# Kernel tuning notes

Measured on AMD Instinct MI355X. Metric: run time of the kernel, lower is better.

Reference implementation:

```python
import jax, jax.numpy as jnp
import numpy as np

D_MODEL = 768
D_STATE = 64
D_CONV = 4
EXPAND = 2
D_INNER = D_MODEL * EXPAND
BATCH = 2
SEQ = 1024
LN_EPS = 1e-5


def setup_inputs() -> dict:
    key = jax.random.key(0)
    ks = jax.random.split(key, 8)
    s = lambda k, shape, scale=0.02: (jax.random.normal(k, shape, jnp.float32) * scale)
    x = jax.random.normal(ks[0], (BATCH, SEQ, D_MODEL), jnp.float32)
    return {
        "x": x,
        "ln_w": jnp.ones((D_MODEL,), jnp.float32),
        "ln_b": jnp.zeros((D_MODEL,), jnp.float32),
        "in_proj_w": s(ks[1], (D_MODEL, 2 * D_INNER)),            # x @ W, torch Linear weight transposed
        "conv_w": s(ks[2], (D_INNER, 1, D_CONV), 0.1),            # depthwise (O, I/groups=1, K)
        "conv_b": jnp.zeros((D_INNER,), jnp.float32),
        "x_proj_w": s(ks[3], (D_INNER, 2 * D_STATE + 1)),
        "A_log": jnp.log(jnp.arange(1, D_STATE + 1, dtype=jnp.float32)),
        "D": jnp.ones((D_INNER,), jnp.float32),
        "dt_w": s(ks[4], (1, D_INNER), 0.5),
        "dt_b": s(ks[5], (D_INNER,), 0.1),
        "out_proj_w": s(ks[6], (D_INNER, D_MODEL)),
    }


def reference(x, ln_w, ln_b, in_proj_w, conv_w, conv_b, x_proj_w, A_log, D, dt_w, dt_b, out_proj_w):
    residual = x
    # LayerNorm
    mu = jnp.mean(x, axis=-1, keepdims=True)
    var = jnp.mean((x - mu) ** 2, axis=-1, keepdims=True)
    h = (x - mu) * jax.lax.rsqrt(var + LN_EPS) * ln_w + ln_b
    # input projection -> (main, gate)
    xz = h @ in_proj_w                                   # (B, L, 2*d_inner)
    x_main, z = jnp.split(xz, 2, axis=-1)
    # causal depthwise conv1d: torch pads (d_conv-1) both sides then truncates to L == left-pad only
    xc = jax.lax.conv_general_dilated(
        x_main.transpose(0, 2, 1), conv_w,
        window_strides=(1,), padding=[(D_CONV - 1, 0)],
        feature_group_count=D_INNER,
        dimension_numbers=("NCH", "OIH", "NCH"))
    xc = (xc + conv_b[None, :, None]).transpose(0, 2, 1)  # (B, L, d_inner)
    xc = jax.nn.silu(xc)
    # input-dependent SSM params
    proj = xc @ x_proj_w                                  # (B, L, 2*d_state+1)
    Bm = proj[..., :D_STATE]
    Cm = proj[..., D_STATE:2 * D_STATE]
    dt = jax.nn.softplus(proj[..., -1:] @ dt_w + dt_b)    # (B, L, d_inner)
    A = -jnp.exp(A_log)                                   # (d_state,)

    def step(h_prev, inp):
        x_t, dt_t, B_t, C_t = inp                         # (B,d_inner),(B,d_inner),(B,d_state),(B,d_state)
        dA = jnp.exp(A[None, None, :] * dt_t[..., None])  # (B, d_inner, d_state)
        h_new = dA * h_prev + (dt_t * x_t)[..., None] * B_t[:, None, :]
        y_t = jnp.einsum("bds,bs->bd", h_new, C_t)
        return h_new, y_t

    h0 = jnp.zeros((x.shape[0], D_INNER, D_STATE), xc.dtype)
    xs = (xc.transpose(1, 0, 2), dt.transpose(1, 0, 2),
          Bm.transpose(1, 0, 2), Cm.transpose(1, 0, 2))
    _, ys = jax.lax.scan(step, h0, xs)                    # ys: (L, B, d_inner)
    y = ys.transpose(1, 0, 2)
    y = y + D * xc
    y = y * jax.nn.silu(z)
    y = y @ out_proj_w                                    # (B, L, d_model)
    return y + residual
```

## Files before the change

kernel.cpp:

```cpp
#include <hip/hip_runtime.h>
#include <hip/hip_bf16.h>
#include <cstdint>
#include <cstddef>

#define D_MODEL   768
#define D_INNER   1536
#define D_STATE   64
#define NBATCH    2
#define SEQ       1024
#define NROWS     (NBATCH*SEQ)
#define NCHUNK    64
#define TCHUNK    16
#define PROJ_LD   132
#define BD_TOT    (NBATCH*D_INNER)

#define L2E 1.4426950408889634f
#define LN2 0.6931471805599453f

typedef __bf16 bf16x8 __attribute__((ext_vector_type(8)));
typedef float  f32x4  __attribute__((ext_vector_type(4)));

__device__ __forceinline__ float fexp2(float x){ return __builtin_amdgcn_exp2f(x); }
__device__ __forceinline__ float flog2(float x){ return __builtin_amdgcn_logf(x); }
__device__ __forceinline__ float softplus_f(float x){
  float r = LN2 * flog2(1.0f + fexp2(x * L2E));
  return x > 15.0f ? x : r;
}
__device__ __forceinline__ float silu_f(float x){
  return x / (1.0f + fexp2(-x * L2E));
}

__device__ __forceinline__ void gload_lds16(const void* g, void* l){
  __builtin_amdgcn_global_load_lds(
      (const __attribute__((address_space(1))) void*)g,
      (__attribute__((address_space(3))) void*)l, 16, 0, 0);
}

#define T1_TILES 2304
#define T3_TILES 1152
#define T2_TILES 192
#define TP_TOTAL (T1_TILES+T3_TILES+T2_TILES)

__global__ __launch_bounds__(256) void prep_all_kernel(
    const float* __restrict__ in_proj, const float* __restrict__ out_proj,
    const float* __restrict__ x_proj, const float* __restrict__ x,
    const float* __restrict__ ln_w, const float* __restrict__ ln_b,
    __bf16* __restrict__ WT1, __bf16* __restrict__ WT3,
    __bf16* __restrict__ WT2, __bf16* __restrict__ h_ln){
  __shared__ float shbuf[32*33];
  const int blk = blockIdx.x;
  if (blk < TP_TOTAL){
    const float* W; __bf16* WT; int K, ldw, tiles_x, idx;
    if (blk < T1_TILES){ W = in_proj; WT = WT1; K = D_MODEL; ldw = 2*D_INNER; tiles_x = 96; idx = blk; }
    else if (blk < T1_TILES+T3_TILES){ W = out_proj; WT = WT3; K = D_INNER; ldw = D_MODEL; tiles_x = 24; idx = blk - T1_TILES; }
    else { W = x_proj; WT = WT2; K = D_INNER; ldw = 129; tiles_x = 4; idx = blk - T1_TILES - T3_TILES; }
    const int n0 = (idx % tiles_x) * 32, k0 = (idx / tiles_x) * 32;
    const int tx = threadIdx.x, ty = threadIdx.y;
    float (*tile)[33] = (float(*)[33])shbuf;
    #pragma unroll
    for (int i = ty; i < 32; i += 8)
      tile[i][tx] = W[(size_t)(k0 + i) * ldw + n0 + tx];
    __syncthreads();
    #pragma unroll
    for (int i = ty; i < 32; i += 8)
      WT[(size_t)(n0 + i) * K + k0 + tx] = (__bf16)tile[tx][i];
  } else {
    const int row = blk - TP_TOTAL;
    const float* xr = x + (size_t)row * D_MODEL;
    const int tid = threadIdx.y * 32 + threadIdx.x;
    float v0 = xr[tid], v1 = xr[tid+256], v2 = xr[tid+512];
    float s  = v0+v1+v2;
    float ss = v0*v0+v1*v1+v2*v2;
    #pragma unroll
    for (int off = 32; off > 0; off >>= 1){
      s  += __shfl_down(s, off);
      ss += __shfl_down(ss, off);
    }
    float* red = shbuf;
    const int wv = tid >> 6, ln = tid & 63;
    if (ln == 0){ red[wv] = s; red[4+wv] = ss; }
    __syncthreads();
    if (tid == 0){
      float S  = red[0]+red[1]+red[2]+red[3];
      float SS = red[4]+red[5]+red[6]+red[7];
      float mu = S * (1.0f/D_MODEL);
      float var = SS * (1.0f/D_MODEL) - mu*mu;
      red[0] = mu;
      red[1] = rsqrtf(var + 1e-5f);
    }
    __syncthreads();
    float mu = red[0], inv = red[1];
    __bf16* orow = h_ln + (size_t)row * D_MODEL;
    orow[tid]     = (__bf16)((v0 - mu)*inv*ln_w[tid]     + ln_b[tid]);
    orow[tid+256] = (__bf16)((v1 - mu)*inv*ln_w[tid+256] + ln_b[tid+256]);
    orow[tid+512] = (__bf16)((v2 - mu)*inv*ln_w[tid+512] + ln_b[tid+512]);
  }
}

struct SMem {
  __bf16 sA[128][32];
  __bf16 sB[128][32];
};

template<int MODE>
__device__ __forceinline__ void gemm_tile(
    const __bf16* __restrict__ A, const __bf16* __restrict__ Bt,
    float* __restrict__ C,
    int lda, int ldb, int ldc, int m0, int n0, int kbeg, int kend,
    SMem& sm, int tid){
  const int wave = tid >> 6;
  const int lane = tid & 63;
  const int quad = lane >> 4;
  const int l16  = lane & 15;
  const int wm = (wave >> 1) * 64;
  const int wn = (wave & 1) * 64;
  const int srow = lane >> 2;
  const int scol = (lane & 3) * 8;

  f32x4 acc[4][4] = {};
  for (int k0 = kbeg; k0 < kend; k0 += 32){
    #pragma unroll
    for (int p = 0; p < 2; ++p){
      int r = wave*32 + p*16 + srow;
      gload_lds16(A  + (size_t)(m0 + r)*lda + k0 + scol, &sm.sA[wave*32 + p*16][0]);
      gload_lds16(Bt + (size_t)(n0 + r)*ldb + k0 + scol, &sm.sB[wave*32 + p*16][0]);
    }
    __syncthreads();
    bf16x8 af[4], bfr[4];
    #pragma unroll
    for (int i = 0; i < 4; ++i) af[i]  = *(const bf16x8*)&sm.sA[wm + i*16 + l16][quad*8];
    #pragma unroll
    for (int j = 0; j < 4; ++j) bfr[j] = *(const bf16x8*)&sm.sB[wn + j*16 + l16][quad*8];
    #pragma unroll
    for (int i = 0; i < 4; ++i)
      #pragma unroll
      for (int j = 0; j < 4; ++j)
        acc[i][j] = __builtin_amdgcn_mfma_f32_16x16x32_bf16(af[i], bfr[j], acc[i][j], 0, 0, 0);
    __syncthreads();
  }
  #pragma unroll
  for (int i = 0; i < 4; ++i)
    #pragma unroll
    for (int j = 0; j < 4; ++j)
      #pragma unroll
      for (int r = 0; r < 4; ++r){
        int row = m0 + wm + i*16 + quad*4 + r;
        int col = n0 + wn + j*16 + l16;
        size_t off = (size_t)row * ldc + col;
        if (MODE == 2) atomicAdd(&C[off], acc[i][j][r]);
        else           C[off] = acc[i][j][r];
      }
}

struct Args {
  const __bf16* h_ln; const __bf16* WT1; const __bf16* WT2; const __bf16* WT3;
  const float* conv_w; const float* conv_b; const float* x_proj;
  const float* dt_w; const float* dt_b; const float* Dp; const float* x;
  float* xz; float* xc; __bf16* xcb; float* proj;
  float* dtv; float* dtx;
  float* sdtA; __bf16* Lb; __bf16* ybf; float* out;
};

__global__ __launch_bounds__(256) void k_gemm1(Args a){
  __shared__ SMem sm;
  gemm_tile<0>(a.h_ln, a.WT1, a.xz, D_MODEL, D_MODEL, 2*D_INNER,
               blockIdx.y*128, blockIdx.x*128, 0, D_MODEL, sm, threadIdx.x);
}

__global__ __launch_bounds__(256) void k_conv(Args a){
  __shared__ float red[4];
  const int row = blockIdx.x;
  const int t   = row & (SEQ-1);
  const int tid = threadIdx.x;
  float vq[6];
  float dtpart = 0.0f;
  #pragma unroll
  for (int q = 0; q < 6; ++q){
    const int d = tid + q*256;
    const float4 w4 = *(const float4*)(a.conv_w + (size_t)d*4);
    float acc = a.conv_b[d];
    if (t >= 3) acc = fmaf(a.xz[(size_t)(row-3)*(2*D_INNER) + d], w4.x, acc);
    if (t >= 2) acc = fmaf(a.xz[(size_t)(row-2)*(2*D_INNER) + d], w4.y, acc);
    if (t >= 1) acc = fmaf(a.xz[(size_t)(row-1)*(2*D_INNER) + d], w4.z, acc);
    acc = fmaf(a.xz[(size_t)row*(2*D_INNER) + d], w4.w, acc);
    float v = silu_f(acc);
    vq[q] = v;
    a.xc[(size_t)row*D_INNER + d]  = v;
    a.xcb[(size_t)row*D_INNER + d] = (__bf16)v;
    dtpart = fmaf(v, a.x_proj[(size_t)d*129 + 128], dtpart);
  }
  #pragma unroll
  for (int off = 32; off > 0; off >>= 1) dtpart += __shfl_down(dtpart, off);
  const int wv = tid >> 6, ln = tid & 63;
  if (ln == 0) red[wv] = dtpart;
  __syncthreads();
  const float draw = red[0]+red[1]+red[2]+red[3];
  #pragma unroll
  for (int q = 0; q < 6; ++q){
    const int d = tid + q*256;
    float dv = softplus_f(fmaf(draw, a.dt_w[d], a.dt_b[d]));
    a.dtv[(size_t)row*D_INNER + d] = dv;
    a.dtx[(size_t)row*D_INNER + d] = dv * vq[q];
  }
  if (tid < 128) a.proj[(size_t)row * PROJ_LD + tid] = 0.0f;
  const float* xr = a.x + (size_t)row * D_MODEL;
  float* orow = a.out + (size_t)row * D_MODEL;
  orow[tid]     = xr[tid];
  orow[tid+256] = xr[tid+256];
  orow[tid+512] = xr[tid+512];
}

__global__ __launch_bounds__(256) void k_xproj(Args a){
  __shared__ SMem sm;
  const int kz = blockIdx.x;
  const int m0 = blockIdx.y * 128;
  gemm_tile<2>(a.xcb, a.WT2, a.proj, D_INNER, D_INNER, PROJ_LD,
               m0, 0, kz*384, kz*384+384, sm, threadIdx.x);
}


__global__ __launch_bounds__(256) void k_scanA(Args a){
  const int half = blockIdx.x & 1;
  const int bd = (blockIdx.x >> 1) * 256 + threadIdx.x;
  const int c  = blockIdx.y;
  const int b  = __builtin_amdgcn_readfirstlane(bd / D_INNER);
  const int d  = bd - b * D_INNER;
  float h[32];
  #pragma unroll
  for (int n = 0; n < 32; ++n) h[n] = 0.0f;
  float sdt = 0.0f;
  #pragma unroll 2
  for (int tl = 0; tl < TCHUNK; ++tl){
    const int row = b*SEQ + c*TCHUNK + tl;
    const float* Brow = a.proj + (size_t)row * PROJ_LD + half*32;
    float dtv = a.dtv[(size_t)row * D_INNER + d];
    float dtx = a.dtx[(size_t)row * D_INNER + d];
    sdt += dtv;
    float r1 = fexp2(-L2E * dtv);
    float r2 = r1*r1, r4 = r2*r2, r8 = r4*r4;
    float r16 = r8*r8, r32 = r16*r16;
    float base = half ? r32 : 1.0f;
    float p0=r1*base, p1=r2*base, p2=r1*r2*base, p3=r4*base,
          p4=r1*r4*base, p5=r2*r4*base, p6=r1*r2*r4*base, p7=r8*base;
    #pragma unroll
    for (int n = 0; n < 32; n += 8){
      h[n]   = fmaf(p0, h[n],   dtx * Brow[n]);
      h[n+1] = fmaf(p1, h[n+1], dtx * Brow[n+1]);
      h[n+2] = fmaf(p2, h[n+2], dtx * Brow[n+2]);
      h[n+3] = fmaf(p3, h[n+3], dtx * Brow[n+3]);
      h[n+4] = fmaf(p4, h[n+4], dtx * Brow[n+4]);
      h[n+5] = fmaf(p5, h[n+5], dtx * Brow[n+5]);
      h[n+6] = fmaf(p6, h[n+6], dtx * Brow[n+6]);
      h[n+7] = fmaf(p7, h[n+7], dtx * Brow[n+7]);
      if (n + 8 < 32){
        p0*=r8; p1*=r8; p2*=r8; p3*=r8; p4*=r8; p5*=r8; p6*=r8; p7*=r8;
      }
    }
  }
  if (half == 0) a.sdtA[(size_t)c * BD_TOT + bd] = sdt;
  #pragma unroll
  for (int n = 0; n < 32; ++n)
    a.Lb[((size_t)c * D_STATE + half*32 + n) * BD_TOT + bd] = (__bf16)h[n];
}

__global__ __launch_bounds__(256) void k_scanB(Args a){
  const int bd = blockIdx.x * 256 + threadIdx.x;
  const int n  = blockIdx.y;
  const float k2n = -(float)(n+1) * L2E;
  float h = 0.0f;
  #pragma unroll 4
  for (int c = 0; c < NCHUNK; ++c){
    float sdt = a.sdtA[(size_t)c * BD_TOT + bd];
    float P = fexp2(k2n * sdt);
    size_t adr = ((size_t)c * D_STATE + n) * BD_TOT + bd;
    float L = (float)a.Lb[adr];
    a.Lb[adr] = (__bf16)h;
    h = fmaf(P, h, L);
  }
}

__global__ __launch_bounds__(256) void k_scanC(Args a){
  const int bd = blockIdx.x * 256 + threadIdx.x;
  const int c  = blockIdx.y;
  const int b  = __builtin_amdgcn_readfirstlane(bd / D_INNER);
  const int d  = bd - b * D_INNER;
  const float Dd = a.Dp[d];
  float h[D_STATE];
  #pragma unroll
  for (int n = 0; n < D_STATE; ++n)
    h[n] = (float)a.Lb[((size_t)c * D_STATE + n) * BD_TOT + bd];
  #pragma unroll 2
  for (int tl = 0; tl < TCHUNK; ++tl){
    const int row = b*SEQ + c*TCHUNK + tl;
    const float* Brow = a.proj + (size_t)row * PROJ_LD;
    const float* Crow = Brow + D_STATE;
    float dtv = a.dtv[(size_t)row * D_INNER + d];
    float dtx = a.dtx[(size_t)row * D_INNER + d];
    float xcv = a.xc[(size_t)row * D_INNER + d];
    float r1 = fexp2(-L2E * dtv);
    float r2 = r1*r1, r4 = r2*r2, r8 = r4*r4;
    float p0=r1, p1=r2, p2=r1*r2, p3=r4, p4=r1*r4, p5=r2*r4, p6=r1*r2*r4, p7=r8;
    float y0=0.f, y1=0.f, y2=0.f, y3=0.f;
    #pragma unroll
    for (int n = 0; n < D_STATE; n += 8){
      h[n]   = fmaf(p0, h[n],   dtx * Brow[n]);   y0 = fmaf(h[n],   Crow[n],   y0);
      h[n+1] = fmaf(p1, h[n+1], dtx * Brow[n+1]); y1 = fmaf(h[n+1], Crow[n+1], y1);
      h[n+2] = fmaf(p2, h[n+2], dtx * Brow[n+2]); y2 = fmaf(h[n+2], Crow[n+2], y2);
      h[n+3] = fmaf(p3, h[n+3], dtx * Brow[n+3]); y3 = fmaf(h[n+3], Crow[n+3], y3);
      h[n+4] = fmaf(p4, h[n+4], dtx * Brow[n+4]); y0 = fmaf(h[n+4], Crow[n+4], y0);
      h[n+5] = fmaf(p5, h[n+5], dtx * Brow[n+5]); y1 = fmaf(h[n+5], Crow[n+5], y1);
      h[n+6] = fmaf(p6, h[n+6], dtx * Brow[n+6]); y2 = fmaf(h[n+6], Crow[n+6], y2);
      h[n+7] = fmaf(p7, h[n+7], dtx * Brow[n+7]); y3 = fmaf(h[n+7], Crow[n+7], y3);
      if (n + 8 < D_STATE){
        p0*=r8; p1*=r8; p2*=r8; p3*=r8; p4*=r8; p5*=r8; p6*=r8; p7*=r8;
      }
    }
    float y = (y0 + y1) + (y2 + y3);
    float zv = a.xz[(size_t)row * (2*D_INNER) + D_INNER + d];
    float yv = (y + Dd * xcv) * silu_f(zv);
    a.ybf[(size_t)row * D_INNER + d] = (__bf16)yv;
  }
}

__global__ __launch_bounds__(256) void k_gemm2(Args a){
  __shared__ SMem sm;
  const int kz = blockIdx.x & 3;
  const int n0 = (blockIdx.x >> 2) * 128;
  const int m0 = blockIdx.y * 128;
  gemm_tile<2>(a.ybf, a.WT3, a.out, D_INNER, D_INNER, D_MODEL,
               m0, n0, kz*384, kz*384+384, sm, threadIdx.x);
}

extern "C" void kernel_launch(void* const* d_in, const int* in_sizes, int n_in,
                              void* d_out, int out_size, void* d_ws, size_t ws_size,
                              hipStream_t stream){
  const float* x        = (const float*)d_in[0];
  const float* ln_w     = (const float*)d_in[1];
  const float* ln_b     = (const float*)d_in[2];
  const float* in_proj  = (const float*)d_in[3];
  const float* conv_w   = (const float*)d_in[4];
  const float* conv_b   = (const float*)d_in[5];
  const float* x_proj   = (const float*)d_in[6];
  const float* A_log    = (const float*)d_in[7];  (void)A_log;
  const float* Dp       = (const float*)d_in[8];
  const float* dt_w     = (const float*)d_in[9];
  const float* dt_b     = (const float*)d_in[10];
  const float* out_proj = (const float*)d_in[11];
  float* out = (float*)d_out;

  char* p = (char*)d_ws;
  size_t used = 0;
  auto alloc = [&](size_t bytes) -> char* {
    char* r = p + used;
    used += (bytes + 255) & ~(size_t)255;
    return r;
  };
  __bf16* h_ln = (__bf16*)alloc((size_t)NROWS*D_MODEL*sizeof(__bf16));
  __bf16* WT1  = (__bf16*)alloc((size_t)(2*D_INNER)*D_MODEL*sizeof(__bf16));
  __bf16* WT3  = (__bf16*)alloc((size_t)D_MODEL*D_INNER*sizeof(__bf16));
  __bf16* WT2  = (__bf16*)alloc((size_t)128*D_INNER*sizeof(__bf16));
  __bf16* ybf  = (__bf16*)alloc((size_t)NROWS*D_INNER*sizeof(__bf16));
  __bf16* xcb  = (__bf16*)alloc((size_t)NROWS*D_INNER*sizeof(__bf16));
  float*  xz   = (float*)alloc((size_t)NROWS*2*D_INNER*sizeof(float));
  float*  xc   = (float*)alloc((size_t)NROWS*D_INNER*sizeof(float));
  float*  proj = (float*)alloc((size_t)NROWS*PROJ_LD*sizeof(float));
  float*  dtv  = (float*)alloc((size_t)NROWS*D_INNER*sizeof(float));
  float*  dtx  = (float*)alloc((size_t)NROWS*D_INNER*sizeof(float));
  float*  sdtA = (float*)alloc((size_t)NCHUNK*BD_TOT*sizeof(float));
  __bf16* Lb   = (__bf16*)alloc((size_t)NCHUNK*D_STATE*BD_TOT*sizeof(__bf16));
  if (used > ws_size) return;

  Args a;
  a.h_ln = h_ln; a.WT1 = WT1; a.WT2 = WT2; a.WT3 = WT3;
  a.conv_w = conv_w; a.conv_b = conv_b; a.x_proj = x_proj;
  a.dt_w = dt_w; a.dt_b = dt_b; a.Dp = Dp; a.x = x;
  a.xz = xz; a.xc = xc; a.xcb = xcb; a.proj = proj;
  a.dtv = dtv; a.dtx = dtx; a.sdtA = sdtA; a.Lb = Lb; a.ybf = ybf; a.out = out;

  hipLaunchKernelGGL(prep_all_kernel, dim3(TP_TOTAL + NROWS), dim3(32,8), 0, stream,
                     in_proj, out_proj, x_proj, x, ln_w, ln_b, WT1, WT3, WT2, h_ln);
  hipLaunchKernelGGL(k_gemm1, dim3(24, 16), dim3(256), 0, stream, a);
  hipLaunchKernelGGL(k_conv,  dim3(NROWS),  dim3(256), 0, stream, a);
  hipLaunchKernelGGL(k_xproj, dim3(4, 16),  dim3(256), 0, stream, a);
  hipLaunchKernelGGL(k_scanA, dim3(24, NCHUNK), dim3(256), 0, stream, a);
  hipLaunchKernelGGL(k_scanB, dim3(12, D_STATE), dim3(256), 0, stream, a);
  hipLaunchKernelGGL(k_scanC, dim3(12, NCHUNK), dim3(256), 0, stream, a);
  hipLaunchKernelGGL(k_gemm2, dim3(24, 16), dim3(256), 0, stream, a);
}
```

Measured before the change: 250.7 us.

## Cut intermediate traffic: bf16 gate, multi-row conv, fewer longer scan chunks

The input GEMM now writes the x branch as fp32 and the gate z as bf16 into separate buffers, and the fp32 xc copy is dropped. The scan reads xc and z as bf16. The conv kernel processes 4 rows per block with a sliding register window and preloads its weights once. The residual copy and proj zeroing move into the prep kernel, which also gathers the dt column of x_proj. The scan switches to 32 chunks of 32 steps, with each scanA thread holding all 64 states in 128-thread blocks. These changes reduce memory traffic and per-row overhead, at the cost of higher register pressure and fewer blocks in the scan, plus bf16 rounding of z and xc.

```diff
diff --git a/kernel.cpp b/kernel.cpp
--- a/kernel.cpp
+++ b/kernel.cpp
@@ -9,10 +9,11 @@
 #define NBATCH    2
 #define SEQ       1024
 #define NROWS     (NBATCH*SEQ)
-#define NCHUNK    64
-#define TCHUNK    16
+#define NCHUNK    32
+#define TCHUNK    32
 #define PROJ_LD   132
 #define BD_TOT    (NBATCH*D_INNER)
+#define RPB       4
 
 #define L2E 1.4426950408889634f
 #define LN2 0.6931471805599453f
@@ -46,7 +47,9 @@
     const float* __restrict__ x_proj, const float* __restrict__ x,
     const float* __restrict__ ln_w, const float* __restrict__ ln_b,
     __bf16* __restrict__ WT1, __bf16* __restrict__ WT3,
-    __bf16* __restrict__ WT2, __bf16* __restrict__ h_ln){
+    __bf16* __restrict__ WT2, __bf16* __restrict__ h_ln,
+    float* __restrict__ proj, float* __restrict__ out,
+    float* __restrict__ wdtc){
   __shared__ float shbuf[32*33];
   const int blk = blockIdx.x;
   if (blk < TP_TOTAL){
@@ -64,7 +67,7 @@
     #pragma unroll
     for (int i = ty; i < 32; i += 8)
       WT[(size_t)(n0 + i) * K + k0 + tx] = (__bf16)tile[tx][i];
-  } else {
+  } else if (blk < TP_TOTAL + NROWS){
     const int row = blk - TP_TOTAL;
     const float* xr = x + (size_t)row * D_MODEL;
     const int tid = threadIdx.y * 32 + threadIdx.x;
@@ -94,6 +97,18 @@
     orow[tid]     = (__bf16)((v0 - mu)*inv*ln_w[tid]     + ln_b[tid]);
     orow[tid+256] = (__bf16)((v1 - mu)*inv*ln_w[tid+256] + ln_b[tid+256]);
     orow[tid+512] = (__bf16)((v2 - mu)*inv*ln_w[tid+512] + ln_b[tid+512]);
+    float* og = out + (size_t)row * D_MODEL;
+    og[tid]     = v0;
+    og[tid+256] = v1;
+    og[tid+512] = v2;
+    if (tid < 128) proj[(size_t)row * PROJ_LD + tid] = 0.0f;
+  } else {
+    const int tid = threadIdx.y * 32 + threadIdx.x;
+    #pragma unroll
+    for (int k = 0; k < 6; ++k){
+      int d = tid + k*256;
+      wdtc[d] = x_proj[(size_t)d*129 + 128];
+    }
   }
 }
 
@@ -105,7 +120,7 @@
 template<int MODE>
 __device__ __forceinline__ void gemm_tile(
     const __bf16* __restrict__ A, const __bf16* __restrict__ Bt,
-    float* __restrict__ C,
+    float* __restrict__ Cf, __bf16* __restrict__ Cb,
     int lda, int ldb, int ldc, int m0, int n0, int kbeg, int kend,
     SMem& sm, int tid){
   const int wave = tid >> 6;
@@ -147,103 +162,119 @@
         int row = m0 + wm + i*16 + quad*4 + r;
         int col = n0 + wn + j*16 + l16;
         size_t off = (size_t)row * ldc + col;
-        if (MODE == 2) atomicAdd(&C[off], acc[i][j][r]);
-        else           C[off] = acc[i][j][r];
+        if (MODE == 2)      atomicAdd(&Cf[off], acc[i][j][r]);
+        else if (MODE == 1) Cb[off] = (__bf16)acc[i][j][r];
+        else                Cf[off] = acc[i][j][r];
       }
 }
 
 struct Args {
   const __bf16* h_ln; const __bf16* WT1; const __bf16* WT2; const __bf16* WT3;
-  const float* conv_w; const float* conv_b; const float* x_proj;
-  const float* dt_w; const float* dt_b; const float* Dp; const float* x;
-  float* xz; float* xc; __bf16* xcb; float* proj;
+  const float* conv_w; const float* conv_b;
+  const float* dt_w; const float* dt_b; const float* Dp;
+  const float* wdtc;
+  float* xz;
+  __bf16* zb;
+  __bf16* xcb; float* proj;
   float* dtv; float* dtx;
   float* sdtA; __bf16* Lb; __bf16* ybf; float* out;
 };
 
 __global__ __launch_bounds__(256) void k_gemm1(Args a){
   __shared__ SMem sm;
-  gemm_tile<0>(a.h_ln, a.WT1, a.xz, D_MODEL, D_MODEL, 2*D_INNER,
-               blockIdx.y*128, blockIdx.x*128, 0, D_MODEL, sm, threadIdx.x);
+  const int bx = blockIdx.x;
+  if (bx < 12)
+    gemm_tile<0>(a.h_ln, a.WT1, a.xz, nullptr, D_MODEL, D_MODEL, D_INNER,
+                 blockIdx.y*128, bx*128, 0, D_MODEL, sm, threadIdx.x);
+  else
+    gemm_tile<1>(a.h_ln, a.WT1 + (size_t)D_INNER*D_MODEL, nullptr, a.zb,
+                 D_MODEL, D_MODEL, D_INNER,
+                 blockIdx.y*128, (bx-12)*128, 0, D_MODEL, sm, threadIdx.x);
 }
 
 __global__ __launch_bounds__(256) void k_conv(Args a){
   __shared__ float red[4];
-  const int row = blockIdx.x;
-  const int t   = row & (SEQ-1);
+  const int r0  = blockIdx.x * RPB;
   const int tid = threadIdx.x;
-  float vq[6];
-  float dtpart = 0.0f;
+  const int t0  = r0 & (SEQ-1);
+  float4 w4[6]; float cb[6], wdt[6], dw[6], db[6];
+  float x1[6], x2[6], x3[6];
   #pragma unroll
   for (int q = 0; q < 6; ++q){
     const int d = tid + q*256;
-    const float4 w4 = *(const float4*)(a.conv_w + (size_t)d*4);
-    float acc = a.conv_b[d];
-    if (t >= 3) acc = fmaf(a.xz[(size_t)(row-3)*(2*D_INNER) + d], w4.x, acc);
-    if (t >= 2) acc = fmaf(a.xz[(size_t)(row-2)*(2*D_INNER) + d], w4.y, acc);
-    if (t >= 1) acc = fmaf(a.xz[(size_t)(row-1)*(2*D_INNER) + d], w4.z, acc);
-    acc = fmaf(a.xz[(size_t)row*(2*D_INNER) + d], w4.w, acc);
-    float v = silu_f(acc);
-    vq[q] = v;
-    a.xc[(size_t)row*D_INNER + d]  = v;
-    a.xcb[(size_t)row*D_INNER + d] = (__bf16)v;
-    dtpart = fmaf(v, a.x_proj[(size_t)d*129 + 128], dtpart);
-  }
-  #pragma unroll
-  for (int off = 32; off > 0; off >>= 1) dtpart += __shfl_down(dtpart, off);
-  const int wv = tid >> 6, ln = tid & 63;
-  if (ln == 0) red[wv] = dtpart;
-  __syncthreads();
-  const float draw = red[0]+red[1]+red[2]+red[3];
-  #pragma unroll
-  for (int q = 0; q < 6; ++q){
-    const int d = tid + q*256;
-    float dv = softplus_f(fmaf(draw, a.dt_w[d], a.dt_b[d]));
-    a.dtv[(size_t)row*D_INNER + d] = dv;
-    a.dtx[(size_t)row*D_INNER + d] = dv * vq[q];
-  }
-  if (tid < 128) a.proj[(size_t)row * PROJ_LD + tid] = 0.0f;
-  const float* xr = a.x + (size_t)row * D_MODEL;
-  float* orow = a.out + (size_t)row * D_MODEL;
-  orow[tid]     = xr[tid];
-  orow[tid+256] = xr[tid+256];
-  orow[tid+512] = xr[tid+512];
+    w4[q]  = *(const float4*)(a.conv_w + (size_t)d*4);
+    cb[q]  = a.conv_b[d];
+    wdt[q] = a.wdtc[d];
+    dw[q]  = a.dt_w[d];
+    db[q]  = a.dt_b[d];
+    x1[q] = (t0 >= 1) ? a.xz[(size_t)(r0-1)*D_INNER + d] : 0.0f;
+    x2[q] = (t0 >= 2) ? a.xz[(size_t)(r0-2)*D_INNER + d] : 0.0f;
+    x3[q] = (t0 >= 3) ? a.xz[(size_t)(r0-3)*D_INNER + d] : 0.0f;
+  }
+  for (int tl = 0; tl < RPB; ++tl){
+    const int row = r0 + tl;
+    float v[6]; float dtpart = 0.0f;
+    #pragma unroll
+    for (int q = 0; q < 6; ++q){
+      const int d = tid + q*256;
+      float x0 = a.xz[(size_t)row*D_INNER + d];
+      float acc = cb[q];
+      acc = fmaf(x3[q], w4[q].x, acc);
+      acc = fmaf(x2[q], w4[q].y, acc);
+      acc = fmaf(x1[q], w4[q].z, acc);
+      acc = fmaf(x0,    w4[q].w, acc);
+      float vv = silu_f(acc);
+      v[q] = vv;
+      a.xcb[(size_t)row*D_INNER + d] = (__bf16)vv;
+      dtpart = fmaf(vv, wdt[q], dtpart);
+      x3[q] = x2[q]; x2[q] = x1[q]; x1[q] = x0;
+    }
+    #pragma unroll
+    for (int off = 32; off > 0; off >>= 1) dtpart += __shfl_down(dtpart, off);
+    if ((tid & 63) == 0) red[tid >> 6] = dtpart;
+    __syncthreads();
+    const float draw = red[0]+red[1]+red[2]+red[3];
+    __syncthreads();
+    #pragma unroll
+    for (int q = 0; q < 6; ++q){
+      const int d = tid + q*256;
+      float dv = softplus_f(fmaf(draw, dw[q], db[q]));
+      a.dtv[(size_t)row*D_INNER + d] = dv;
+      a.dtx[(size_t)row*D_INNER + d] = dv * v[q];
+    }
+  }
 }
 
 __global__ __launch_bounds__(256) void k_xproj(Args a){
   __shared__ SMem sm;
   const int kz = blockIdx.x;
   const int m0 = blockIdx.y * 128;
-  gemm_tile<2>(a.xcb, a.WT2, a.proj, D_INNER, D_INNER, PROJ_LD,
+  gemm_tile<2>(a.xcb, a.WT2, a.proj, nullptr, D_INNER, D_INNER, PROJ_LD,
                m0, 0, kz*384, kz*384+384, sm, threadIdx.x);
 }
 
 
-__global__ __launch_bounds__(256) void k_scanA(Args a){
-  const int half = blockIdx.x & 1;
-  const int bd = (blockIdx.x >> 1) * 256 + threadIdx.x;
+__global__ __launch_bounds__(128) void k_scanA(Args a){
+  const int bd = blockIdx.x * 128 + threadIdx.x;
   const int c  = blockIdx.y;
   const int b  = __builtin_amdgcn_readfirstlane(bd / D_INNER);
   const int d  = bd - b * D_INNER;
-  float h[32];
+  float h[D_STATE];
   #pragma unroll
-  for (int n = 0; n < 32; ++n) h[n] = 0.0f;
+  for (int n = 0; n < D_STATE; ++n) h[n] = 0.0f;
   float sdt = 0.0f;
   #pragma unroll 2
   for (int tl = 0; tl < TCHUNK; ++tl){
     const int row = b*SEQ + c*TCHUNK + tl;
-    const float* Brow = a.proj + (size_t)row * PROJ_LD + half*32;
+    const float* Brow = a.proj + (size_t)row * PROJ_LD;
     float dtv = a.dtv[(size_t)row * D_INNER + d];
     float dtx = a.dtx[(size_t)row * D_INNER + d];
     sdt += dtv;
     float r1 = fexp2(-L2E * dtv);
     float r2 = r1*r1, r4 = r2*r2, r8 = r4*r4;
-    float r16 = r8*r8, r32 = r16*r16;
-    float base = half ? r32 : 1.0f;
-    float p0=r1*base, p1=r2*base, p2=r1*r2*base, p3=r4*base,
-          p4=r1*r4*base, p5=r2*r4*base, p6=r1*r2*r4*base, p7=r8*base;
-    #pragma unroll
-    for (int n = 0; n < 32; n += 8){
+    float p0=r1, p1=r2, p2=r1*r2, p3=r4, p4=r1*r4, p5=r2*r4, p6=r1*r2*r4, p7=r8;
+    #pragma unroll
+    for (int n = 0; n < D_STATE; n += 8){
       h[n]   = fmaf(p0, h[n],   dtx * Brow[n]);
       h[n+1] = fmaf(p1, h[n+1], dtx * Brow[n+1]);
       h[n+2] = fmaf(p2, h[n+2], dtx * Brow[n+2]);
@@ -252,15 +283,15 @@
       h[n+5] = fmaf(p5, h[n+5], dtx * Brow[n+5]);
       h[n+6] = fmaf(p6, h[n+6], dtx * Brow[n+6]);
       h[n+7] = fmaf(p7, h[n+7], dtx * Brow[n+7]);
-      if (n + 8 < 32){
+      if (n + 8 < D_STATE){
         p0*=r8; p1*=r8; p2*=r8; p3*=r8; p4*=r8; p5*=r8; p6*=r8; p7*=r8;
       }
     }
   }
-  if (half == 0) a.sdtA[(size_t)c * BD_TOT + bd] = sdt;
+  a.sdtA[(size_t)c * BD_TOT + bd] = sdt;
   #pragma unroll
-  for (int n = 0; n < 32; ++n)
-    a.Lb[((size_t)c * D_STATE + half*32 + n) * BD_TOT + bd] = (__bf16)h[n];
+  for (int n = 0; n < D_STATE; ++n)
+    a.Lb[((size_t)c * D_STATE + n) * BD_TOT + bd] = (__bf16)h[n];
 }
 
 __global__ __launch_bounds__(256) void k_scanB(Args a){
@@ -279,8 +310,8 @@
   }
 }
 
-__global__ __launch_bounds__(256) void k_scanC(Args a){
-  const int bd = blockIdx.x * 256 + threadIdx.x;
+__global__ __launch_bounds__(128) void k_scanC(Args a){
+  const int bd = blockIdx.x * 128 + threadIdx.x;
   const int c  = blockIdx.y;
   const int b  = __builtin_amdgcn_readfirstlane(bd / D_INNER);
   const int d  = bd - b * D_INNER;
@@ -296,7 +327,7 @@
     const float* Crow = Brow + D_STATE;
     float dtv = a.dtv[(size_t)row * D_INNER + d];
     float dtx = a.dtx[(size_t)row * D_INNER + d];
-    float xcv = a.xc[(size_t)row * D_INNER + d];
+    float xcv = (float)a.xcb[(size_t)row * D_INNER + d];
     float r1 = fexp2(-L2E * dtv);
     float r2 = r1*r1, r4 = r2*r2, r8 = r4*r4;
     float p0=r1, p1=r2, p2=r1*r2, p3=r4, p4=r1*r4, p5=r2*r4, p6=r1*r2*r4, p7=r8;
@@ -316,7 +347,7 @@
       }
     }
     float y = (y0 + y1) + (y2 + y3);
-    float zv = a.xz[(size_t)row * (2*D_INNER) + D_INNER + d];
+    float zv = (float)a.zb[(size_t)row * D_INNER + d];
     float yv = (y + Dd * xcv) * silu_f(zv);
     a.ybf[(size_t)row * D_INNER + d] = (__bf16)yv;
   }
@@ -327,7 +358,7 @@
   const int kz = blockIdx.x & 3;
   const int n0 = (blockIdx.x >> 2) * 128;
   const int m0 = blockIdx.y * 128;
-  gemm_tile<2>(a.ybf, a.WT3, a.out, D_INNER, D_INNER, D_MODEL,
+  gemm_tile<2>(a.ybf, a.WT3, a.out, nullptr, D_INNER, D_INNER, D_MODEL,
                m0, n0, kz*384, kz*384+384, sm, threadIdx.x);
 }
 
@@ -361,29 +392,31 @@
   __bf16* WT2  = (__bf16*)alloc((size_t)128*D_INNER*sizeof(__bf16));
   __bf16* ybf  = (__bf16*)alloc((size_t)NROWS*D_INNER*sizeof(__bf16));
   __bf16* xcb  = (__bf16*)alloc((size_t)NROWS*D_INNER*sizeof(__bf16));
-  float*  xz   = (float*)alloc((size_t)NROWS*2*D_INNER*sizeof(float));
-  float*  xc   = (float*)alloc((size_t)NROWS*D_INNER*sizeof(float));
+  __bf16* zb   = (__bf16*)alloc((size_t)NROWS*D_INNER*sizeof(__bf16));
+  float*  xz   = (float*)alloc((size_t)NROWS*D_INNER*sizeof(float));
   float*  proj = (float*)alloc((size_t)NROWS*PROJ_LD*sizeof(float));
   float*  dtv  = (float*)alloc((size_t)NROWS*D_INNER*sizeof(float));
   float*  dtx  = (float*)alloc((size_t)NROWS*D_INNER*sizeof(float));
   float*  sdtA = (float*)alloc((size_t)NCHUNK*BD_TOT*sizeof(float));
+  float*  wdtc = (float*)alloc((size_t)D_INNER*sizeof(float));
   __bf16* Lb   = (__bf16*)alloc((size_t)NCHUNK*D_STATE*BD_TOT*sizeof(__bf16));
   if (used > ws_size) return;
 
   Args a;
   a.h_ln = h_ln; a.WT1 = WT1; a.WT2 = WT2; a.WT3 = WT3;
-  a.conv_w = conv_w; a.conv_b = conv_b; a.x_proj = x_proj;
-  a.dt_w = dt_w; a.dt_b = dt_b; a.Dp = Dp; a.x = x;
-  a.xz = xz; a.xc = xc; a.xcb = xcb; a.proj = proj;
+  a.conv_w = conv_w; a.conv_b = conv_b;
+  a.dt_w = dt_w; a.dt_b = dt_b; a.Dp = Dp; a.wdtc = wdtc;
+  a.xz = xz; a.zb = zb; a.xcb = xcb; a.proj = proj;
   a.dtv = dtv; a.dtx = dtx; a.sdtA = sdtA; a.Lb = Lb; a.ybf = ybf; a.out = out;
 
-  hipLaunchKernelGGL(prep_all_kernel, dim3(TP_TOTAL + NROWS), dim3(32,8), 0, stream,
-                     in_proj, out_proj, x_proj, x, ln_w, ln_b, WT1, WT3, WT2, h_ln);
+  hipLaunchKernelGGL(prep_all_kernel, dim3(TP_TOTAL + NROWS + 1), dim3(32,8), 0, stream,
+                     in_proj, out_proj, x_proj, x, ln_w, ln_b, WT1, WT3, WT2, h_ln,
+                     proj, out, wdtc);
   hipLaunchKernelGGL(k_gemm1, dim3(24, 16), dim3(256), 0, stream, a);
-  hipLaunchKernelGGL(k_conv,  dim3(NROWS),  dim3(256), 0, stream, a);
+  hipLaunchKernelGGL(k_conv,  dim3(NROWS/RPB), dim3(256), 0, stream, a);
   hipLaunchKernelGGL(k_xproj, dim3(4, 16),  dim3(256), 0, stream, a);
-  hipLaunchKernelGGL(k_scanA, dim3(24, NCHUNK), dim3(256), 0, stream, a);
+  hipLaunchKernelGGL(k_scanA, dim3(24, NCHUNK), dim3(128), 0, stream, a);
   hipLaunchKernelGGL(k_scanB, dim3(12, D_STATE), dim3(256), 0, stream, a);
-  hipLaunchKernelGGL(k_scanC, dim3(12, NCHUNK), dim3(256), 0, stream, a);
+  hipLaunchKernelGGL(k_scanC, dim3(24, NCHUNK), dim3(128), 0, stream, a);
   hipLaunchKernelGGL(k_gemm2, dim3(24, 16), dim3(256), 0, stream, a);
 }
```

Result: no change. 252.0 us (+0.5%).
